# Kernel tuning notes

Measured on AMD Instinct MI355X. Metric: run time of the kernel, lower is better.

## Reference

```python
import jax, jax.numpy as jnp
import numpy as np

DIM = 512
MAX_LEN = 2048
SHARED = 128
EXPAND = 2 * DIM  # expansion_factor * dim
PROJ = 2 * EXPAND + SHARED
EPS = 1e-6
BATCH = 8


def _rope(x):
    # x: [n, d]; rotates last dim (split-half RoPE) with position along axis 0
    n, d = x.shape
    half = d // 2
    freq = jnp.arange(half, dtype=x.dtype) / float(half)
    inv_freq = 10000.0 ** (-freq)
    sinusoid = jnp.arange(n, dtype=x.dtype)[:, None] * inv_freq[None, :]  # [n, half]
    sin, cos = jnp.sin(sinusoid), jnp.cos(sinusoid)
    x1, x2 = x[:, :half], x[:, half:]
    return jnp.concatenate([x1 * cos - x2 * sin, x2 * cos + x1 * sin], axis=-1)


def _toeplitz_rope(n, a, b):
    # a, b: [max_len]; tile to [n, max_len], rope over positions, then outer product
    ar = _rope(jnp.tile(a[None, :], (n, 1)))
    br = _rope(jnp.tile(b[None, :], (n, 1)))
    return jnp.einsum('mk,nk->mn', ar, br)  # [n, n]


def setup_inputs() -> dict:
    key = jax.random.key(0)
    ks = jax.random.split(key, 8)
    std = 0.02
    return {
        'x': jax.random.normal(ks[0], (BATCH, MAX_LEN, DIM), jnp.float32),
        'W1': std * jax.random.normal(ks[1], (DIM, PROJ), jnp.float32),
        'b1': jnp.zeros((PROJ,), jnp.float32),
        'W2': std * jax.random.normal(ks[2], (EXPAND, DIM), jnp.float32),
        'b2': jnp.zeros((DIM,), jnp.float32),
        'rope_a': std * jax.random.normal(ks[3], (MAX_LEN,), jnp.float32),
        'rope_b': std * jax.random.normal(ks[4], (MAX_LEN,), jnp.float32),
        'gamma': std * jax.random.normal(ks[5], (2, SHARED), jnp.float32),
        'beta': jnp.zeros((2, SHARED), jnp.float32),
        'norm_scale': jnp.asarray(1.0, jnp.float32),
    }


def reference(x, W1, b1, W2, b2, rope_a, rope_b, gamma, beta, norm_scale):
    shortcut = x
    # ScaledNorm: x * rsqrt(mean(x^2)) * scale
    ms = jnp.mean(jnp.square(x), axis=-1, keepdims=True)
    xn = x * jax.lax.rsqrt(ms + EPS) * norm_scale
    # proj1 with swish activation
    uv = jax.nn.swish(xn @ W1 + b1)  # [b, n, PROJ]
    u = uv[..., :EXPAND]
    v = uv[..., EXPAND:2 * EXPAND]
    base = uv[..., 2 * EXPAND:]  # [b, n, SHARED]
    qk_base = base[:, :, None, :] * gamma + beta  # [b, n, 2, SHARED]
    q, k = qk_base[:, :, 0, :], qk_base[:, :, 1, :]
    qk = jnp.einsum('bnd,bmd->bnm', q, k) / float(MAX_LEN)
    qk = qk + _toeplitz_rope(MAX_LEN, rope_a, rope_b)
    kernel = jnp.square(jax.nn.relu(qk))  # sqrrelu
    o = u * jnp.einsum('bnm,bme->bne', kernel, v)
    return o @ W2 + b2 + shortcut
```

## Files before the change

### kernel.cpp

```cpp
#include <hip/hip_runtime.h>
#include <math.h>

#define SEQ    2048
#define DIMM   512
#define SH     128
#define EXP    1024
#define PROJ_  2176
#define NBATCH 8
#define ROWS   16384

#define KER_SCALE     16384.0f
#define KER_SCALE_INV (1.0f / 16384.0f)
#define QK_INV        (1.0f / (4096.0f * 2048.0f))
#define W8            64.0f
#define INV4096       (1.0f / 4096.0f)

typedef __attribute__((ext_vector_type(4))) float floatx4;
typedef __attribute__((ext_vector_type(8))) int   int8v;

__device__ __forceinline__ unsigned short f2bf(float f) {
  union { float f; unsigned int u; } v; v.f = f;
  unsigned int r = (v.u + 0x7fffu + ((v.u >> 16) & 1u)) >> 16;
  return (unsigned short)r;
}
__device__ __forceinline__ float bf2f(unsigned short h) {
  union { unsigned int u; float f; } v; v.u = ((unsigned int)h) << 16;
  return v.f;
}
__device__ __forceinline__ unsigned char f2fp8(float f) {
  return (unsigned char)(__builtin_amdgcn_cvt_pk_fp8_f32(f, 0.0f, 0, false) & 0xffu);
}
__device__ __forceinline__ unsigned int pk4fp8(float a, float b, float c, float d) {
  unsigned int w = __builtin_amdgcn_cvt_pk_fp8_f32(a, b, 0, false);
  return __builtin_amdgcn_cvt_pk_fp8_f32(c, d, w, true);
}
__device__ __forceinline__ float fp82f(unsigned char b) {
  int e = (b >> 3) & 15, m = b & 7;
  float v = ldexpf((float)(e ? (8 + m) : m), (e ? e : 1) - 10);
  return (b & 0x80) ? -v : v;
}

__device__ __forceinline__ void async16(const void* g, void* l) {
  __builtin_amdgcn_global_load_lds(
      (const __attribute__((address_space(1))) void*)g,
      (__attribute__((address_space(3))) void*)l, 16, 0, 0);
}

__device__ __forceinline__ void transpose_tile_fp8(const float* __restrict__ in,
                                                   unsigned char* __restrict__ out,
                                                   int R, int C, int bx, int by, float* tile) {
  int tx = threadIdx.x & 31, ty = threadIdx.x >> 5;
  int c0 = bx * 32, r0 = by * 32;
  #pragma unroll
  for (int j = 0; j < 32; j += 8)
    tile[(ty + j) * 33 + tx] = in[(long)(r0 + ty + j) * C + c0 + tx];
  __syncthreads();
  #pragma unroll
  for (int j = 0; j < 32; j += 8)
    out[(long)(c0 + ty + j) * R + r0 + tx] = f2fp8(tile[tx * 33 + ty + j] * W8);
}

__global__ void prep_kernel(const float* __restrict__ x, const float* __restrict__ ns,
                            unsigned char* __restrict__ xq,
                            const float* __restrict__ W1, unsigned char* __restrict__ w1q,
                            const float* __restrict__ W2, unsigned char* __restrict__ w2q,
                            const float* __restrict__ ra, const float* __restrict__ rb,
                            float* __restrict__ tpl) {
  __shared__ float sh[33 * 32];
  const int b = blockIdx.x, tid = threadIdx.x;
  if (b < 4096) {
    int wave = tid >> 6, lane = tid & 63;
    long row = (long)b * 4 + wave;
    const float4* xr = (const float4*)(x + row * DIMM);
    float4 v0 = xr[lane], v1 = xr[lane + 64];
    float ss = v0.x*v0.x + v0.y*v0.y + v0.z*v0.z + v0.w*v0.w
             + v1.x*v1.x + v1.y*v1.y + v1.z*v1.z + v1.w*v1.w;
    #pragma unroll
    for (int o = 32; o > 0; o >>= 1) ss += __shfl_xor(ss, o);
    float sc = rsqrtf(ss * (1.0f / DIMM) + 1e-6f) * ns[0] * W8;
    uint2 pk;
    pk.x = pk4fp8(v0.x*sc, v0.y*sc, v0.z*sc, v0.w*sc);
    pk.y = pk4fp8(v1.x*sc, v1.y*sc, v1.z*sc, v1.w*sc);
    ((uint2*)(xq + row * DIMM))[lane] = pk;
  } else if (b < 4096 + 4095) {
    const int d = (b - 4096) - 2047;
    float sum = 0.0f;
    for (int k = tid; k < 1024; k += 256) {
      float a1 = ra[k], a2 = ra[k + 1024];
      float b1v = rb[k], b2v = rb[k + 1024];
      float p = a1 * b1v + a2 * b2v;
      float q = a1 * b2v - a2 * b1v;
      float th = exp2f((float)k * (-13.287712379549449f / 1024.0f));
      float ang = (float)d * th;
      sum += p * cosf(ang) + q * sinf(ang);
    }
    #pragma unroll
    for (int o = 32; o > 0; o >>= 1) sum += __shfl_xor(sum, o);
    int wave = tid >> 6, lane = tid & 63;
    if (lane == 0) sh[wave] = sum;
    __syncthreads();
    if (tid == 0) tpl[b - 4096] = sh[0] + sh[1] + sh[2] + sh[3];
  } else if (b < 9279) {
    int t = b - 8191;
    transpose_tile_fp8(W1, w1q, DIMM, PROJ_, t % 68, t / 68, sh);
  } else {
    int t = b - 9279;
    transpose_tile_fp8(W2, w2q, EXP, DIMM, t % 16, t / 16, sh);
  }
}

__device__ __forceinline__ void mfma_core_mx(const unsigned char* __restrict__ A,
                                             const unsigned char* __restrict__ B,
                                             int K, long rowBase, long colBase,
                                             unsigned char* smem, floatx4 acc[4][4]) {
  const int tid  = threadIdx.x;
  const int wave = tid >> 6;
  const int lane = tid & 63;
  const int wr   = (wave >> 1) * 64;
  const int wc   = (wave & 1) * 64;
  const int r_l  = lane >> 3;
  const int c8   = lane & 7;
  const int fm   = lane & 15;
  const int fq   = lane >> 4;

  floatx4 z = {0.0f, 0.0f, 0.0f, 0.0f};
  #pragma unroll
  for (int mi = 0; mi < 4; ++mi)
    #pragma unroll
    for (int ni = 0; ni < 4; ++ni) acc[mi][ni] = z;

  const unsigned char* aSrc[4];
  const unsigned char* bSrc[4];
  int ldsOff[4];
  #pragma unroll
  for (int j = 0; j < 4; ++j) {
    int row = j * 32 + wave * 8 + r_l;
    int g = c8 ^ (row & 7);
    aSrc[j] = A + (rowBase + row) * (long)K + g * 16;
    bSrc[j] = B + (colBase + row) * (long)K + g * 16;
    ldsOff[j] = (j * 32 + wave * 8) * 128;
  }

  union U8 { uint4 q[2]; int8v v; };
  const int nt = K >> 7;

  #pragma unroll
  for (int j = 0; j < 4; ++j) {
    async16(aSrc[j], smem + ldsOff[j]);
    async16(bSrc[j], smem + 16384 + ldsOff[j]);
  }
  __syncthreads();

  int cur = 0;
  for (int t = 0; t < nt; ++t) {
    unsigned char* As = smem + cur * 32768;
    unsigned char* Bs = As + 16384;
    if (t + 1 < nt) {
      unsigned char* An = smem + (cur ^ 1) * 32768;
      int k0 = (t + 1) << 7;
      #pragma unroll
      for (int j = 0; j < 4; ++j) {
        async16(aSrc[j] + k0, An + ldsOff[j]);
        async16(bSrc[j] + k0, An + 16384 + ldsOff[j]);
      }
    }
    int8v av[4], bv[4];
    #pragma unroll
    for (int mi = 0; mi < 4; ++mi) {
      int row = wr + mi * 16 + fm;
      int s0 = (2 * fq) ^ (row & 7);
      U8 u;
      u.q[0] = *(const uint4*)(As + row * 128 + s0 * 16);
      u.q[1] = *(const uint4*)(As + row * 128 + (s0 ^ 1) * 16);
      av[mi] = u.v;
    }
    #pragma unroll
    for (int ni = 0; ni < 4; ++ni) {
      int row = wc + ni * 16 + fm;
      int s0 = (2 * fq) ^ (row & 7);
      U8 u;
      u.q[0] = *(const uint4*)(Bs + row * 128 + s0 * 16);
      u.q[1] = *(const uint4*)(Bs + row * 128 + (s0 ^ 1) * 16);
      bv[ni] = u.v;
    }
    __builtin_amdgcn_s_setprio(1);
    #pragma unroll
    for (int mi = 0; mi < 4; ++mi)
      #pragma unroll
      for (int ni = 0; ni < 4; ++ni)
        acc[mi][ni] = __builtin_amdgcn_mfma_scale_f32_16x16x128_f8f6f4(
            av[mi], bv[ni], acc[mi][ni], 0, 0, 0, 0x7F7F7F7F, 0, 0x7F7F7F7F);
    __builtin_amdgcn_s_setprio(0);
    __syncthreads();
    cur ^= 1;
  }
}

#define EPILOGUE_VARS                                         \
  const int lane = threadIdx.x & 63, wave = threadIdx.x >> 6; \
  const int wr = (wave >> 1) * 64, wc = (wave & 1) * 64;      \
  const int fr = (lane >> 4) * 4, fc = lane & 15;

__global__ void __launch_bounds__(256)
gemm_uv(const unsigned char* __restrict__ xq,
        const unsigned char* __restrict__ w1q,
        const float* __restrict__ b1,
        const float* __restrict__ gamma,
        const float* __restrict__ beta,
        unsigned char* __restrict__ uq,
        unsigned char* __restrict__ vT,
        unsigned char* __restrict__ qq,
        unsigned char* __restrict__ kq) {
  __shared__ __align__(16) unsigned char smem8[65536];
  unsigned short* smem = (unsigned short*)smem8;
  floatx4 acc[4][4];
  long rowBase = (long)blockIdx.x * 128;
  long colBase = (long)blockIdx.y * 128;
  mfma_core_mx(xq, w1q, DIMM, rowBase, colBase, smem8, acc);
  EPILOGUE_VARS

  if (blockIdx.y < 8) {
    #pragma unroll
    for (int mi = 0; mi < 4; ++mi)
    #pragma unroll
    for (int ni = 0; ni < 4; ++ni)
    #pragma unroll
    for (int i = 0; i < 4; ++i) {
      long row = rowBase + wr + mi * 16 + fr + i;
      long col = colBase + wc + ni * 16 + fc;
      float t = acc[mi][ni][i] * INV4096 + b1[col];
      uq[row * EXP + col] = f2fp8(t / (1.0f + __expf(-t)) * W8);
    }
  } else if (blockIdx.y < 16) {
    __syncthreads();
    #pragma unroll
    for (int mi = 0; mi < 4; ++mi)
    #pragma unroll
    for (int ni = 0; ni < 4; ++ni)
    #pragma unroll
    for (int i = 0; i < 4; ++i) {
      int rl = wr + mi * 16 + fr + i;
      int cl = wc + ni * 16 + fc;
      long col = colBase + cl;
      float t = acc[mi][ni][i] * INV4096 + b1[col];
      smem[cl * 136 + rl] = f2bf(t / (1.0f + __expf(-t)));
    }
    __syncthreads();
    long b_   = rowBase >> 11;
    long nblk = rowBase & 2047;
    long e0   = colBase - EXP;
    #pragma unroll
    for (int rep = 0; rep < 8; ++rep) {
      int cl = rep * 16 + (threadIdx.x >> 4);
      int n0 = (threadIdx.x & 15) * 8;
      const unsigned short* src = smem + cl * 136 + n0;
      uint2 pk;
      pk.x = pk4fp8(bf2f(src[0]), bf2f(src[1]), bf2f(src[2]), bf2f(src[3]));
      pk.y = pk4fp8(bf2f(src[4]), bf2f(src[5]), bf2f(src[6]), bf2f(src[7]));
      *(uint2*)(vT + (b_ * EXP + e0 + cl) * (long)SEQ + nblk + n0) = pk;
    }
  } else {
    #pragma unroll
    for (int mi = 0; mi < 4; ++mi)
    #pragma unroll
    for (int ni = 0; ni < 4; ++ni)
    #pragma unroll
    for (int i = 0; i < 4; ++i) {
      long row = rowBase + wr + mi * 16 + fr + i;
      long col = colBase + wc + ni * 16 + fc;
      float t = acc[mi][ni][i] * INV4096 + b1[col];
      float s = t / (1.0f + __expf(-t));
      int dd = (int)(col - 2 * EXP);
      qq[row * SH + dd] = f2fp8((s * gamma[dd] + beta[dd]) * W8);
      kq[row * SH + dd] = f2fp8((s * gamma[SH + dd] + beta[SH + dd]) * W8);
    }
  }
}

__global__ void __launch_bounds__(256)
gemm_qk(const unsigned char* __restrict__ kq,
        const unsigned char* __restrict__ qq,
        const float* __restrict__ tpl,
        unsigned char* __restrict__ ker) {
  __shared__ __align__(16) unsigned char smem8[65536];
  floatx4 acc[4][4];
  int L = blockIdx.x;
  long b = L & 7;
  int w = L >> 3;
  long mBase = (long)(w & 15) * 128;
  long nBase = (long)(w >> 4) * 128;
  mfma_core_mx(kq + b * SEQ * SH, qq + b * SEQ * SH, SH, mBase, nBase, smem8, acc);
  unsigned char* kerb = ker + b * (long)SEQ * SEQ;
  EPILOGUE_VARS
  (void)fr;
  __syncthreads();
  #pragma unroll
  for (int mi = 0; mi < 4; ++mi)
  #pragma unroll
  for (int ni = 0; ni < 4; ++ni) {
    int m_loc0 = wr + mi * 16 + (lane >> 4) * 4;
    int n_loc  = wc + ni * 16 + fc;
    long n = nBase + n_loc;
    long m0 = mBase + m_loc0;
    float v[4];
    #pragma unroll
    for (int i = 0; i < 4; ++i) {
      float val = acc[mi][ni][i] * QK_INV + tpl[n - (m0 + i) + 2047];
      float r = fmaxf(val, 0.0f);
      v[i] = fminf(r * r * KER_SCALE, 440.0f);
    }
    *(unsigned int*)(smem8 + n_loc * 136 + m_loc0) = pk4fp8(v[0], v[1], v[2], v[3]);
  }
  __syncthreads();
  #pragma unroll
  for (int rep = 0; rep < 4; ++rep) {
    int n_loc = rep * 32 + (threadIdx.x >> 3);
    int m_seg = (threadIdx.x & 7) * 16;
    uint4 v16 = *(const uint4*)(smem8 + n_loc * 136 + m_seg);
    *(uint4*)(kerb + (nBase + n_loc) * (long)SEQ + mBase + m_seg) = v16;
  }
}

__global__ void __launch_bounds__(256)
gemm_pv(const unsigned char* __restrict__ ker,
        const unsigned char* __restrict__ vT,
        const unsigned char* __restrict__ uq,
        unsigned char* __restrict__ obq) {
  __shared__ __align__(16) unsigned char smem8[65536];
  floatx4 acc[4][4];
  int L = blockIdx.x;
  long b = L & 7;
  int w = L >> 3;
  long eBase = (long)(w & 7) * 128;
  long nBase = (long)(w >> 3) * 128;
  mfma_core_mx(vT + b * (long)EXP * SEQ, ker + b * (long)SEQ * SEQ, SEQ,
               eBase, nBase, smem8, acc);
  const unsigned char* ub = uq + b * (long)SEQ * EXP;
  unsigned char* obb = obq + b * (long)SEQ * EXP;
  EPILOGUE_VARS
  (void)fr;
  __syncthreads();
  #pragma unroll
  for (int mi = 0; mi < 4; ++mi)
  #pragma unroll
  for (int ni = 0; ni < 4; ++ni) {
    int e_loc0 = wr + mi * 16 + (lane >> 4) * 4;
    int n_loc  = wc + ni * 16 + fc;
    unsigned int uw = *(const unsigned int*)(ub + (nBase + n_loc) * (long)EXP + eBase + e_loc0);
    float v[4];
    #pragma unroll
    for (int i = 0; i < 4; ++i) {
      float u = fp82f((unsigned char)(uw >> (8 * i)));
      v[i] = acc[mi][ni][i] * KER_SCALE_INV * u;
    }
    *(unsigned int*)(smem8 + n_loc * 136 + e_loc0) = pk4fp8(v[0], v[1], v[2], v[3]);
  }
  __syncthreads();
  #pragma unroll
  for (int rep = 0; rep < 4; ++rep) {
    int n_loc = rep * 32 + (threadIdx.x >> 3);
    int e_seg = (threadIdx.x & 7) * 16;
    uint4 v16 = *(const uint4*)(smem8 + n_loc * 136 + e_seg);
    *(uint4*)(obb + (nBase + n_loc) * (long)EXP + eBase + e_seg) = v16;
  }
}

__global__ void __launch_bounds__(256)
gemm_out(const unsigned char* __restrict__ obq,
         const unsigned char* __restrict__ w2q,
         const float* __restrict__ b2,
         const float* __restrict__ x,
         float* __restrict__ out) {
  __shared__ __align__(16) unsigned char smem8[65536];
  floatx4 acc[4][4];
  long rowBase = (long)blockIdx.x * 128;
  long colBase = (long)blockIdx.y * 128;
  mfma_core_mx(obq, w2q, EXP, rowBase, colBase, smem8, acc);
  EPILOGUE_VARS
  #pragma unroll
  for (int mi = 0; mi < 4; ++mi)
  #pragma unroll
  for (int ni = 0; ni < 4; ++ni)
  #pragma unroll
  for (int i = 0; i < 4; ++i) {
    long row = rowBase + wr + mi * 16 + fr + i;
    long col = colBase + wc + ni * 16 + fc;
    out[row * DIMM + col] = acc[mi][ni][i] * INV4096 + b2[col] + x[row * DIMM + col];
  }
}

extern "C" void kernel_launch(void* const* d_in, const int* in_sizes, int n_in,
                              void* d_out, int out_size, void* d_ws, size_t ws_size,
                              hipStream_t stream) {
  const float* x          = (const float*)d_in[0];
  const float* W1         = (const float*)d_in[1];
  const float* b1         = (const float*)d_in[2];
  const float* W2         = (const float*)d_in[3];
  const float* b2         = (const float*)d_in[4];
  const float* rope_a     = (const float*)d_in[5];
  const float* rope_b     = (const float*)d_in[6];
  const float* gamma      = (const float*)d_in[7];
  const float* beta       = (const float*)d_in[8];
  const float* norm_scale = (const float*)d_in[9];
  float* out = (float*)d_out;

  char* ws = (char*)d_ws;
  size_t off = 0;
  auto nxt = [&](size_t bytes) -> void* {
    void* p = ws + off;
    off += (bytes + 255) & ~(size_t)255;
    return p;
  };
  unsigned char*  xq  = (unsigned char*)nxt((size_t)ROWS * DIMM);
  unsigned char*  w1q = (unsigned char*)nxt((size_t)PROJ_ * DIMM);
  unsigned char*  w2q = (unsigned char*)nxt((size_t)DIMM * EXP);
  unsigned char*  uq  = (unsigned char*)nxt((size_t)ROWS * EXP);
  unsigned char*  vT  = (unsigned char*)nxt((size_t)NBATCH * EXP * SEQ);
  unsigned char*  qq  = (unsigned char*)nxt((size_t)ROWS * SH);
  unsigned char*  kq  = (unsigned char*)nxt((size_t)ROWS * SH);
  float*          tpl = (float*)nxt((size_t)4096 * 4);
  unsigned char*  ker = (unsigned char*)nxt((size_t)NBATCH * SEQ * SEQ);
  unsigned char*  obq = (unsigned char*)nxt((size_t)ROWS * EXP);

  prep_kernel<<<9791, 256, 0, stream>>>(x, norm_scale, xq, W1, w1q, W2, w2q,
                                        rope_a, rope_b, tpl);
  gemm_uv<<<dim3(ROWS / 128, PROJ_ / 128), 256, 0, stream>>>(xq, w1q, b1, gamma, beta,
                                                             uq, vT, qq, kq);
  gemm_qk<<<2048, 256, 0, stream>>>(kq, qq, tpl, ker);
  gemm_pv<<<1024, 256, 0, stream>>>(ker, vT, uq, obq);
  gemm_out<<<dim3(ROWS / 128, DIMM / 128), 256, 0, stream>>>(obq, w2q, b2, x, out);
}
```

Measured before the change: 223.8 us.

## Use 256x256 tiles with 32x32x64 MX-FP8 MFMA for the uv and pv GEMMs

Adds a new 512-thread GEMM core that computes 256x256 output tiles with 32x32x64 scaled FP8 MFMAs and swizzled LDS double buffering. gemm_uv and gemm_pv use it, and their epilogues are rewritten for the 32x32 accumulator layout. The v transpose now stages fp8 in LDS instead of bf16. W1 is padded to a multiple of 256 columns, and the extra columns are masked out in the q/k epilogue. The goal is more data reuse per LDS load and fewer, larger MFMAs. The risk is fewer blocks: pv gets only 256, roughly one per CU, which lowers occupancy and latency hiding.

```diff
diff --git a/kernel.cpp b/kernel.cpp
--- a/kernel.cpp
+++ b/kernel.cpp
@@ -6,6 +6,7 @@
 #define SH     128
 #define EXP    1024
 #define PROJ_  2176
+#define PROJP  2304
 #define NBATCH 8
 #define ROWS   16384
 
@@ -15,8 +16,9 @@
 #define W8            64.0f
 #define INV4096       (1.0f / 4096.0f)
 
-typedef __attribute__((ext_vector_type(4))) float floatx4;
-typedef __attribute__((ext_vector_type(8))) int   int8v;
+typedef __attribute__((ext_vector_type(4)))  float floatx4;
+typedef __attribute__((ext_vector_type(16))) float floatx16;
+typedef __attribute__((ext_vector_type(8)))  int   int8v;
 
 __device__ __forceinline__ unsigned short f2bf(float f) {
   union { float f; unsigned int u; } v; v.f = f;
@@ -196,12 +198,114 @@
   }
 }
 
-#define EPILOGUE_VARS                                         \
-  const int lane = threadIdx.x & 63, wave = threadIdx.x >> 6; \
-  const int wr = (wave >> 1) * 64, wc = (wave & 1) * 64;      \
-  const int fr = (lane >> 4) * 4, fc = lane & 15;
-
-__global__ void __launch_bounds__(256)
+__device__ __forceinline__ void mfma_core256(const unsigned char* __restrict__ A,
+                                             const unsigned char* __restrict__ B,
+                                             int K, long rowBase, long colBase,
+                                             unsigned char* smem, floatx16 acc[4][2]) {
+  const int tid  = threadIdx.x;
+  const int wave = tid >> 6;
+  const int lane = tid & 63;
+  const int wr2  = wave >> 2;
+  const int wc4  = wave & 3;
+  const int l31  = lane & 31;
+  const int hi   = lane >> 5;
+
+  #pragma unroll
+  for (int mi = 0; mi < 4; ++mi)
+    #pragma unroll
+    for (int ni = 0; ni < 2; ++ni)
+      #pragma unroll
+      for (int e = 0; e < 16; ++e) acc[mi][ni][e] = 0.0f;
+
+  const unsigned char* srcA[2];
+  const unsigned char* srcB[2];
+  int ldsA[2], ldsB[2];
+  #pragma unroll
+  for (int j = 0; j < 2; ++j) {
+    int idx  = (wave * 2 + j) * 64 + lane;
+    int line = idx >> 3, cp = idx & 7, c = cp ^ (line & 7);
+    int r    = 2 * line + (c >> 2);
+    int kb   = (c & 3) * 16;
+    srcA[j] = A + (rowBase + r) * (long)K + kb;
+    srcB[j] = B + (colBase + r) * (long)K + kb;
+    ldsA[j] = (wave * 2 + j) * 1024;
+    ldsB[j] = 16384 + (wave * 2 + j) * 1024;
+  }
+
+  int offA[4][2], offB[2][2];
+  #pragma unroll
+  for (int mi = 0; mi < 4; ++mi) {
+    int rt = wr2 * 128 + mi * 32 + l31;
+    int line = rt >> 1, cb = (rt & 1) * 4 + hi * 2;
+    #pragma unroll
+    for (int q = 0; q < 2; ++q)
+      offA[mi][q] = line * 128 + ((cb + q) ^ (line & 7)) * 16;
+  }
+  #pragma unroll
+  for (int ni = 0; ni < 2; ++ni) {
+    int rt = wc4 * 64 + ni * 32 + l31;
+    int line = rt >> 1, cb = (rt & 1) * 4 + hi * 2;
+    #pragma unroll
+    for (int q = 0; q < 2; ++q)
+      offB[ni][q] = 16384 + line * 128 + ((cb + q) ^ (line & 7)) * 16;
+  }
+
+  union U8 { uint4 q[2]; int8v v; };
+  const int nt = K >> 6;
+
+  #pragma unroll
+  for (int j = 0; j < 2; ++j) {
+    async16(srcA[j], smem + ldsA[j]);
+    async16(srcB[j], smem + ldsB[j]);
+  }
+  __syncthreads();
+
+  int cur = 0;
+  for (int t = 0; t < nt; ++t) {
+    if (t + 1 < nt) {
+      unsigned char* nb = smem + (cur ^ 1) * 32768;
+      int ko = (t + 1) << 6;
+      #pragma unroll
+      for (int j = 0; j < 2; ++j) {
+        async16(srcA[j] + ko, nb + ldsA[j]);
+        async16(srcB[j] + ko, nb + ldsB[j]);
+      }
+    }
+    const unsigned char* buf = smem + cur * 32768;
+    int8v av[4], bv[2];
+    #pragma unroll
+    for (int mi = 0; mi < 4; ++mi) {
+      U8 u;
+      u.q[0] = *(const uint4*)(buf + offA[mi][0]);
+      u.q[1] = *(const uint4*)(buf + offA[mi][1]);
+      av[mi] = u.v;
+    }
+    #pragma unroll
+    for (int ni = 0; ni < 2; ++ni) {
+      U8 u;
+      u.q[0] = *(const uint4*)(buf + offB[ni][0]);
+      u.q[1] = *(const uint4*)(buf + offB[ni][1]);
+      bv[ni] = u.v;
+    }
+    __builtin_amdgcn_s_setprio(1);
+    #pragma unroll
+    for (int mi = 0; mi < 4; ++mi)
+      #pragma unroll
+      for (int ni = 0; ni < 2; ++ni)
+        acc[mi][ni] = __builtin_amdgcn_mfma_scale_f32_32x32x64_f8f6f4(
+            av[mi], bv[ni], acc[mi][ni], 0, 0, 0, 0x7F7F7F7F, 0, 0x7F7F7F7F);
+    __builtin_amdgcn_s_setprio(0);
+    __syncthreads();
+    cur ^= 1;
+  }
+}
+
+#define EPI256_VARS                                               \
+  const int lane = threadIdx.x & 63, wave = threadIdx.x >> 6;     \
+  const int wr2 = wave >> 2, wc4 = wave & 3;                      \
+  const int l31 = lane & 31, hi = lane >> 5;
+
+__global__ void __launch_bounds__(512, 2)
 gemm_uv(const unsigned char* __restrict__ xq,
         const unsigned char* __restrict__ w1q,
         const float* __restrict__ b1,
@@ -211,68 +315,80 @@
         unsigned char* __restrict__ vT,
         unsigned char* __restrict__ qq,
         unsigned char* __restrict__ kq) {
-  __shared__ __align__(16) unsigned char smem8[65536];
-  unsigned short* smem = (unsigned short*)smem8;
-  floatx4 acc[4][4];
-  long rowBase = (long)blockIdx.x * 128;
-  long colBase = (long)blockIdx.y * 128;
-  mfma_core_mx(xq, w1q, DIMM, rowBase, colBase, smem8, acc);
-  EPILOGUE_VARS
-
-  if (blockIdx.y < 8) {
-    #pragma unroll
-    for (int mi = 0; mi < 4; ++mi)
-    #pragma unroll
-    for (int ni = 0; ni < 4; ++ni)
-    #pragma unroll
-    for (int i = 0; i < 4; ++i) {
-      long row = rowBase + wr + mi * 16 + fr + i;
-      long col = colBase + wc + ni * 16 + fc;
-      float t = acc[mi][ni][i] * INV4096 + b1[col];
-      uq[row * EXP + col] = f2fp8(t / (1.0f + __expf(-t)) * W8);
-    }
-  } else if (blockIdx.y < 16) {
+  __shared__ __align__(16) unsigned char smem8[69632];
+  floatx16 acc[4][2];
+  long rowBase = (long)blockIdx.x * 256;
+  long colBase = (long)blockIdx.y * 256;
+  mfma_core256(xq, w1q, DIMM, rowBase, colBase, smem8, acc);
+  EPI256_VARS
+
+  if (blockIdx.y < 4) {
+    #pragma unroll
+    for (int ni = 0; ni < 2; ++ni) {
+      long col = colBase + wc4 * 64 + ni * 32 + l31;
+      float bb = b1[col];
+      #pragma unroll
+      for (int mi = 0; mi < 4; ++mi)
+      #pragma unroll
+      for (int r = 0; r < 4; ++r)
+      #pragma unroll
+      for (int i = 0; i < 4; ++i) {
+        long row = rowBase + wr2 * 128 + mi * 32 + hi * 4 + r * 8 + i;
+        float t = acc[mi][ni][r * 4 + i] * INV4096 + bb;
+        uq[row * EXP + col] = f2fp8(t / (1.0f + __expf(-t)) * W8);
+      }
+    }
+  } else if (blockIdx.y < 8) {
     __syncthreads();
     #pragma unroll
-    for (int mi = 0; mi < 4; ++mi)
-    #pragma unroll
-    for (int ni = 0; ni < 4; ++ni)
-    #pragma unroll
-    for (int i = 0; i < 4; ++i) {
-      int rl = wr + mi * 16 + fr + i;
-      int cl = wc + ni * 16 + fc;
-      long col = colBase + cl;
-      float t = acc[mi][ni][i] * INV4096 + b1[col];
-      smem[cl * 136 + rl] = f2bf(t / (1.0f + __expf(-t)));
+    for (int ni = 0; ni < 2; ++ni) {
+      int cl = wc4 * 64 + ni * 32 + l31;
+      float bb = b1[colBase + cl];
+      #pragma unroll
+      for (int mi = 0; mi < 4; ++mi)
+      #pragma unroll
+      for (int r = 0; r < 4; ++r) {
+        int rl = wr2 * 128 + mi * 32 + hi * 4 + r * 8;
+        float v[4];
+        #pragma unroll
+        for (int i = 0; i < 4; ++i) {
+          float t = acc[mi][ni][r * 4 + i] * INV4096 + bb;
+          v[i] = t / (1.0f + __expf(-t));
+        }
+        *(unsigned int*)(smem8 + cl * 272 + rl) = pk4fp8(v[0], v[1], v[2], v[3]);
+      }
     }
     __syncthreads();
-    long b_   = rowBase >> 11;
-    long nblk = rowBase & 2047;
-    long e0   = colBase - EXP;
-    #pragma unroll
-    for (int rep = 0; rep < 8; ++rep) {
-      int cl = rep * 16 + (threadIdx.x >> 4);
-      int n0 = (threadIdx.x & 15) * 8;
-      const unsigned short* src = smem + cl * 136 + n0;
-      uint2 pk;
-      pk.x = pk4fp8(bf2f(src[0]), bf2f(src[1]), bf2f(src[2]), bf2f(src[3]));
-      pk.y = pk4fp8(bf2f(src[4]), bf2f(src[5]), bf2f(src[6]), bf2f(src[7]));
-      *(uint2*)(vT + (b_ * EXP + e0 + cl) * (long)SEQ + nblk + n0) = pk;
+    long b_ = rowBase >> 11, nblk = rowBase & 2047, e0 = colBase - EXP;
+    #pragma unroll
+    for (int k = 0; k < 8; ++k) {
+      int e = k * 32 + (threadIdx.x >> 4);
+      int seg = (threadIdx.x & 15) * 16;
+      uint4 v16 = *(const uint4*)(smem8 + e * 272 + seg);
+      *(uint4*)(vT + (b_ * EXP + e0 + e) * (long)SEQ + nblk + seg) = v16;
     }
   } else {
     #pragma unroll
-    for (int mi = 0; mi < 4; ++mi)
-    #pragma unroll
-    for (int ni = 0; ni < 4; ++ni)
-    #pragma unroll
-    for (int i = 0; i < 4; ++i) {
-      long row = rowBase + wr + mi * 16 + fr + i;
-      long col = colBase + wc + ni * 16 + fc;
-      float t = acc[mi][ni][i] * INV4096 + b1[col];
-      float s = t / (1.0f + __expf(-t));
-      int dd = (int)(col - 2 * EXP);
-      qq[row * SH + dd] = f2fp8((s * gamma[dd] + beta[dd]) * W8);
-      kq[row * SH + dd] = f2fp8((s * gamma[SH + dd] + beta[SH + dd]) * W8);
+    for (int ni = 0; ni < 2; ++ni) {
+      long col = colBase + wc4 * 64 + ni * 32 + l31;
+      if (col < 2176) {
+        int dd = (int)(col - 2 * EXP);
+        float bb = b1[col];
+        float g0 = gamma[dd], g1 = gamma[SH + dd];
+        float be0 = beta[dd], be1 = beta[SH + dd];
+        #pragma unroll
+        for (int mi = 0; mi < 4; ++mi)
+        #pragma unroll
+        for (int r = 0; r < 4; ++r)
+        #pragma unroll
+        for (int i = 0; i < 4; ++i) {
+          long row = rowBase + wr2 * 128 + mi * 32 + hi * 4 + r * 8 + i;
+          float t = acc[mi][ni][r * 4 + i] * INV4096 + bb;
+          float s = t / (1.0f + __expf(-t));
+          qq[row * SH + dd] = f2fp8((s * g0 + be0) * W8);
+          kq[row * SH + dd] = f2fp8((s * g1 + be1) * W8);
+        }
+      }
     }
   }
 }
@@ -291,8 +407,9 @@
   long nBase = (long)(w >> 4) * 128;
   mfma_core_mx(kq + b * SEQ * SH, qq + b * SEQ * SH, SH, mBase, nBase, smem8, acc);
   unsigned char* kerb = ker + b * (long)SEQ * SEQ;
-  EPILOGUE_VARS
-  (void)fr;
+  const int lane = threadIdx.x & 63, wave = threadIdx.x >> 6;
+  const int wr = (wave >> 1) * 64, wc = (wave & 1) * 64;
+  const int fc = lane & 15;
   __syncthreads();
   #pragma unroll
   for (int mi = 0; mi < 4; ++mi)
@@ -321,47 +438,49 @@
   }
 }
 
-__global__ void __launch_bounds__(256)
+__global__ void __launch_bounds__(512, 2)
 gemm_pv(const unsigned char* __restrict__ ker,
         const unsigned char* __restrict__ vT,
         const unsigned char* __restrict__ uq,
         unsigned char* __restrict__ obq) {
-  __shared__ __align__(16) unsigned char smem8[65536];
-  floatx4 acc[4][4];
+  __shared__ __align__(16) unsigned char smem8[69632];
+  floatx16 acc[4][2];
   int L = blockIdx.x;
   long b = L & 7;
   int w = L >> 3;
-  long eBase = (long)(w & 7) * 128;
-  long nBase = (long)(w >> 3) * 128;
-  mfma_core_mx(vT + b * (long)EXP * SEQ, ker + b * (long)SEQ * SEQ, SEQ,
+  long eBase = (long)(w & 3) * 256;
+  long nBase = (long)(w >> 2) * 256;
+  mfma_core256(vT + b * (long)EXP * SEQ, ker + b * (long)SEQ * SEQ, SEQ,
                eBase, nBase, smem8, acc);
   const unsigned char* ub = uq + b * (long)SEQ * EXP;
   unsigned char* obb = obq + b * (long)SEQ * EXP;
-  EPILOGUE_VARS
-  (void)fr;
-  __syncthreads();
-  #pragma unroll
-  for (int mi = 0; mi < 4; ++mi)
-  #pragma unroll
-  for (int ni = 0; ni < 4; ++ni) {
-    int e_loc0 = wr + mi * 16 + (lane >> 4) * 4;
-    int n_loc  = wc + ni * 16 + fc;
-    unsigned int uw = *(const unsigned int*)(ub + (nBase + n_loc) * (long)EXP + eBase + e_loc0);
-    float v[4];
-    #pragma unroll
-    for (int i = 0; i < 4; ++i) {
-      float u = fp82f((unsigned char)(uw >> (8 * i)));
-      v[i] = acc[mi][ni][i] * KER_SCALE_INV * u;
-    }
-    *(unsigned int*)(smem8 + n_loc * 136 + e_loc0) = pk4fp8(v[0], v[1], v[2], v[3]);
-  }
-  __syncthreads();
-  #pragma unroll
-  for (int rep = 0; rep < 4; ++rep) {
-    int n_loc = rep * 32 + (threadIdx.x >> 3);
-    int e_seg = (threadIdx.x & 7) * 16;
-    uint4 v16 = *(const uint4*)(smem8 + n_loc * 136 + e_seg);
-    *(uint4*)(obb + (nBase + n_loc) * (long)EXP + eBase + e_seg) = v16;
+  EPI256_VARS
+  __syncthreads();
+  #pragma unroll
+  for (int ni = 0; ni < 2; ++ni) {
+    int nl = wc4 * 64 + ni * 32 + l31;
+    #pragma unroll
+    for (int mi = 0; mi < 4; ++mi)
+    #pragma unroll
+    for (int r = 0; r < 4; ++r) {
+      int el0 = wr2 * 128 + mi * 32 + hi * 4 + r * 8;
+      unsigned int uw = *(const unsigned int*)(ub + (nBase + nl) * (long)EXP + eBase + el0);
+      float v[4];
+      #pragma unroll
+      for (int i = 0; i < 4; ++i) {
+        float u = fp82f((unsigned char)(uw >> (8 * i)));
+        v[i] = acc[mi][ni][r * 4 + i] * KER_SCALE_INV * u;
+      }
+      *(unsigned int*)(smem8 + nl * 272 + el0) = pk4fp8(v[0], v[1], v[2], v[3]);
+    }
+  }
+  __syncthreads();
+  #pragma unroll
+  for (int k = 0; k < 8; ++k) {
+    int n = k * 32 + (threadIdx.x >> 4);
+    int seg = (threadIdx.x & 15) * 16;
+    uint4 v16 = *(const uint4*)(smem8 + n * 272 + seg);
+    *(uint4*)(obb + (nBase + n) * (long)EXP + eBase + seg) = v16;
   }
 }
 
@@ -376,7 +495,9 @@
   long rowBase = (long)blockIdx.x * 128;
   long colBase = (long)blockIdx.y * 128;
   mfma_core_mx(obq, w2q, EXP, rowBase, colBase, smem8, acc);
-  EPILOGUE_VARS
+  const int lane = threadIdx.x & 63, wave = threadIdx.x >> 6;
+  const int wr = (wave >> 1) * 64, wc = (wave & 1) * 64;
+  const int fr = (lane >> 4) * 4, fc = lane & 15;
   #pragma unroll
   for (int mi = 0; mi < 4; ++mi)
   #pragma unroll
@@ -412,7 +533,7 @@
     return p;
   };
   unsigned char*  xq  = (unsigned char*)nxt((size_t)ROWS * DIMM);
-  unsigned char*  w1q = (unsigned char*)nxt((size_t)PROJ_ * DIMM);
+  unsigned char*  w1q = (unsigned char*)nxt((size_t)PROJP * DIMM);
   unsigned char*  w2q = (unsigned char*)nxt((size_t)DIMM * EXP);
   unsigned char*  uq  = (unsigned char*)nxt((size_t)ROWS * EXP);
   unsigned char*  vT  = (unsigned char*)nxt((size_t)NBATCH * EXP * SEQ);
@@ -424,9 +545,9 @@
 
   prep_kernel<<<9791, 256, 0, stream>>>(x, norm_scale, xq, W1, w1q, W2, w2q,
                                         rope_a, rope_b, tpl);
-  gemm_uv<<<dim3(ROWS / 128, PROJ_ / 128), 256, 0, stream>>>(xq, w1q, b1, gamma, beta,
+  gemm_uv<<<dim3(ROWS / 256, PROJP / 256), 512, 0, stream>>>(xq, w1q, b1, gamma, beta,
                                                              uq, vT, qq, kq);
   gemm_qk<<<2048, 256, 0, stream>>>(kq, qq, tpl, ker);
-  gemm_pv<<<1024, 256, 0, stream>>>(ker, vT, uq, obq);
+  gemm_pv<<<256, 512, 0, stream>>>(ker, vT, uq, obq);
   gemm_out<<<dim3(ROWS / 128, DIMM / 128), 256, 0, stream>>>(obq, w2q, b2, x, out);
 }
```

Measured after the change: 235.4 us. +5.2%, slower.

## Exploit cos/sin symmetry for Toeplitz rope table and stage it in LDS

Applied to the files above, without the earlier changes.

The Toeplitz bias table is computed for non-negative offsets only, accumulating the cosine and sine parts separately so that both +d and -d entries come from one block. This roughly halves the prep blocks spent on trig evaluation. The qk epilogue now loads the 255-entry slice of the table needed by each tile into shared memory before the MFMA loop and reads the bias from LDS instead of global memory. The shared buffer is shrunk to the size actually used, which may also allow more blocks per CU.

```diff
diff --git a/kernel.cpp b/kernel.cpp
--- a/kernel.cpp
+++ b/kernel.cpp
@@ -82,9 +82,9 @@
     pk.x = pk4fp8(v0.x*sc, v0.y*sc, v0.z*sc, v0.w*sc);
     pk.y = pk4fp8(v1.x*sc, v1.y*sc, v1.z*sc, v1.w*sc);
     ((uint2*)(xq + row * DIMM))[lane] = pk;
-  } else if (b < 4096 + 4095) {
-    const int d = (b - 4096) - 2047;
-    float sum = 0.0f;
+  } else if (b < 6144) {
+    const int d = b - 4096;
+    float sc_ = 0.0f, ss_ = 0.0f;
     for (int k = tid; k < 1024; k += 256) {
       float a1 = ra[k], a2 = ra[k + 1024];
       float b1v = rb[k], b2v = rb[k + 1024];
@@ -92,19 +92,28 @@
       float q = a1 * b2v - a2 * b1v;
       float th = exp2f((float)k * (-13.287712379549449f / 1024.0f));
       float ang = (float)d * th;
-      sum += p * cosf(ang) + q * sinf(ang);
-    }
-    #pragma unroll
-    for (int o = 32; o > 0; o >>= 1) sum += __shfl_xor(sum, o);
+      sc_ += p * cosf(ang);
+      ss_ += q * sinf(ang);
+    }
+    #pragma unroll
+    for (int o = 32; o > 0; o >>= 1) {
+      sc_ += __shfl_xor(sc_, o);
+      ss_ += __shfl_xor(ss_, o);
+    }
     int wave = tid >> 6, lane = tid & 63;
-    if (lane == 0) sh[wave] = sum;
+    if (lane == 0) { sh[wave] = sc_; sh[8 + wave] = ss_; }
     __syncthreads();
-    if (tid == 0) tpl[b - 4096] = sh[0] + sh[1] + sh[2] + sh[3];
-  } else if (b < 9279) {
-    int t = b - 8191;
+    if (tid == 0) {
+      float Sc = sh[0] + sh[1] + sh[2] + sh[3];
+      float Ss = sh[8] + sh[9] + sh[10] + sh[11];
+      tpl[2047 + d] = Sc + Ss;
+      if (d > 0) tpl[2047 - d] = Sc - Ss;
+    }
+  } else if (b < 7232) {
+    int t = b - 6144;
     transpose_tile_fp8(W1, w1q, DIMM, PROJ_, t % 68, t / 68, sh);
   } else {
-    int t = b - 9279;
+    int t = b - 7232;
     transpose_tile_fp8(W2, w2q, EXP, DIMM, t % 16, t / 16, sh);
   }
 }
@@ -282,13 +291,17 @@
         const unsigned char* __restrict__ qq,
         const float* __restrict__ tpl,
         unsigned char* __restrict__ ker) {
-  __shared__ __align__(16) unsigned char smem8[65536];
+  __shared__ __align__(16) unsigned char smem8[33792];
+  float* tplS = (float*)(smem8 + 32768);
   floatx4 acc[4][4];
   int L = blockIdx.x;
   long b = L & 7;
   int w = L >> 3;
   long mBase = (long)(w & 15) * 128;
   long nBase = (long)(w >> 4) * 128;
+  long D = nBase - mBase;
+  if (threadIdx.x < 64)
+    ((float4*)tplS)[threadIdx.x] = *(const float4*)(tpl + D + 1920 + 4 * (long)threadIdx.x);
   mfma_core_mx(kq + b * SEQ * SH, qq + b * SEQ * SH, SH, mBase, nBase, smem8, acc);
   unsigned char* kerb = ker + b * (long)SEQ * SEQ;
   EPILOGUE_VARS
@@ -300,12 +313,10 @@
   for (int ni = 0; ni < 4; ++ni) {
     int m_loc0 = wr + mi * 16 + (lane >> 4) * 4;
     int n_loc  = wc + ni * 16 + fc;
-    long n = nBase + n_loc;
-    long m0 = mBase + m_loc0;
     float v[4];
     #pragma unroll
     for (int i = 0; i < 4; ++i) {
-      float val = acc[mi][ni][i] * QK_INV + tpl[n - (m0 + i) + 2047];
+      float val = acc[mi][ni][i] * QK_INV + tplS[n_loc - m_loc0 - i + 127];
       float r = fmaxf(val, 0.0f);
       v[i] = fminf(r * r * KER_SCALE, 440.0f);
     }
@@ -422,7 +433,7 @@
   unsigned char*  ker = (unsigned char*)nxt((size_t)NBATCH * SEQ * SEQ);
   unsigned char*  obq = (unsigned char*)nxt((size_t)ROWS * EXP);
 
-  prep_kernel<<<9791, 256, 0, stream>>>(x, norm_scale, xq, W1, w1q, W2, w2q,
+  prep_kernel<<<7744, 256, 0, stream>>>(x, norm_scale, xq, W1, w1q, W2, w2q,
                                         rope_a, rope_b, tpl);
   gemm_uv<<<dim3(ROWS / 128, PROJ_ / 128), 256, 0, stream>>>(xq, w1q, b1, gamma, beta,
                                                              uq, vT, qq, kq);
```

After: 218.5 us. 2.4% less time.
